# Performance work log

Hardware: AMD Instinct MI355X
Metric: run time of the kernel (lower is better)

Reference implementation:

```python
import jax, jax.numpy as jnp
import numpy as np

D_MODEL = 1024
NUM_HEADS = 16
D_K = D_MODEL // NUM_HEADS
B, S = 1, 4096


def setup_inputs() -> dict:
    key = jax.random.key(0)
    ks = jax.random.split(key, 11)
    std = 1.0 / np.sqrt(D_MODEL)
    def lin(k):
        kw, kb = jax.random.split(k)
        W = jax.random.uniform(kw, (D_MODEL, D_MODEL), jnp.float32, -std, std)
        b = jax.random.uniform(kb, (D_MODEL,), jnp.float32, -std, std)
        return W, b
    Wq, bq = lin(ks[0]); Wk, bk = lin(ks[1]); Wv, bv = lin(ks[2]); Wo, bo = lin(ks[3])
    q = jax.random.normal(ks[4], (B, S, D_MODEL), jnp.float32)
    k = jax.random.normal(ks[5], (B, S, D_MODEL), jnp.float32)
    v = jax.random.normal(ks[6], (B, S, D_MODEL), jnp.float32)
    return {"q": q, "k": k, "v": v,
            "Wq": Wq, "bq": bq, "Wk": Wk, "bk": bk,
            "Wv": Wv, "bv": bv, "Wo": Wo, "bo": bo}


def reference(q, k, v, Wq, bq, Wk, bk, Wv, bv, Wo, bo):
    Bq, Sq, _ = q.shape
    # Linear projections (torch Linear: x @ W.T + b)
    def split_heads(x):
        return x.reshape(Bq, -1, NUM_HEADS, D_K).transpose(0, 2, 1, 3)  # [B,H,S,Dk]
    query = split_heads(q @ Wq.T + bq)
    key_ = split_heads(k @ Wk.T + bk)
    value = split_heads(v @ Wv.T + bv)
    scores = jnp.einsum('bhsd,bhtd->bhst', query, key_) / jnp.sqrt(jnp.float32(D_K))
    attn = jax.nn.softmax(scores, axis=-1)  # [B,H,S,S]
    ctx = jnp.einsum('bhst,bhtd->bhsd', attn, value)
    ctx = ctx.transpose(0, 2, 1, 3).reshape(Bq, Sq, NUM_HEADS * D_K)
    return ctx @ Wo.T + bo
```

## Files before the change

kernel.cpp:

```cpp
#include <hip/hip_runtime.h>
#include <cstdint>
#include <cstddef>

#define S_LEN 4096
#define DMODEL 1024
#define NHEADS 16
#define DK 64
#define ACT (S_LEN * DMODEL)
#define WELE (DMODEL * DMODEL)

typedef __bf16 bf16;
typedef bf16  bf16x4 __attribute__((ext_vector_type(4)));
typedef bf16  bf16x8 __attribute__((ext_vector_type(8)));
typedef float f32x4  __attribute__((ext_vector_type(4)));

__device__ __forceinline__ void async16(const void* g, void* l) {
    __builtin_amdgcn_global_load_lds(
        (__attribute__((address_space(1))) void*)(uintptr_t)g,
        (__attribute__((address_space(3))) void*)(uintptr_t)l,
        16, 0, 0);
}

__device__ __forceinline__ float fast_exp2(float x) {
#if __has_builtin(__builtin_amdgcn_exp2f)
    return __builtin_amdgcn_exp2f(x);
#else
    return exp2f(x);
#endif
}

__global__ void __launch_bounds__(256) cvt7(
    const float* a0, const float* a1, const float* a2,
    const float* w0, const float* w1, const float* w2, const float* w3,
    bf16* oa0, bf16* oa1, bf16* oa2,
    bf16* ow0, bf16* ow1, bf16* ow2, bf16* ow3,
    int nA, int nB)
{
    const float* s; bf16* d; int n4;
    switch (blockIdx.y) {
        case 0: s = a0; d = oa0; n4 = nA; break;
        case 1: s = a1; d = oa1; n4 = nA; break;
        case 2: s = a2; d = oa2; n4 = nA; break;
        case 3: s = w0; d = ow0; n4 = nB; break;
        case 4: s = w1; d = ow1; n4 = nB; break;
        case 5: s = w2; d = ow2; n4 = nB; break;
        default: s = w3; d = ow3; n4 = nB; break;
    }
    int i = blockIdx.x * 256 + threadIdx.x;
    if (i < n4) {
        float4 v = ((const float4*)s)[i];
        bf16x4 r = { (bf16)v.x, (bf16)v.y, (bf16)v.z, (bf16)v.w };
        ((bf16x4*)d)[i] = r;
    }
}

__device__ __forceinline__ void gemm_core_128x128(
    const bf16* __restrict__ A, const bf16* __restrict__ B,
    bf16* As, bf16* Bs, f32x4 (&acc)[4][4],
    int m0, int n0, int wm, int wn, int K)
{
    const int tid  = threadIdx.x;
    const int wave = tid >> 6;
    const int lane = tid & 63;
    const int quad = lane >> 4;
    const int l16  = lane & 15;

    const int srow = tid >> 2;
    const int scol = (tid & 3) * 8;
    const bf16* Ag = A + (size_t)(m0 + srow) * K + scol;
    const bf16* Bg = B + (size_t)(n0 + srow) * K + scol;
    char* lA = (char*)As + wave * 1024;
    char* lB = (char*)Bs + wave * 1024;

    for (int k0 = 0; k0 < K; k0 += 32) {
        async16(Ag,                  lA);
        async16(Ag + (size_t)64 * K, lA + 4096);
        async16(Bg,                  lB);
        async16(Bg + (size_t)64 * K, lB + 4096);
        Ag += 32; Bg += 32;
        __syncthreads();

        bf16x8 af[4], bfr[4];
#pragma unroll
        for (int i = 0; i < 4; ++i)
            af[i] = *(const bf16x8*)&As[(wm + i * 16 + l16) * 32 + quad * 8];
#pragma unroll
        for (int i = 0; i < 4; ++i)
            bfr[i] = *(const bf16x8*)&Bs[(wn + i * 16 + l16) * 32 + quad * 8];

#pragma unroll
        for (int mi = 0; mi < 4; ++mi)
#pragma unroll
            for (int ni = 0; ni < 4; ++ni)
                acc[mi][ni] = __builtin_amdgcn_mfma_f32_16x16x32_bf16(
                    af[mi], bfr[ni], acc[mi][ni], 0, 0, 0);
        __syncthreads();
    }
}

__global__ void __launch_bounds__(256) proj_qkv(
    const bf16* __restrict__ Xq, const bf16* __restrict__ Wq, const float* __restrict__ bq, bf16* __restrict__ Qo,
    const bf16* __restrict__ Xk, const bf16* __restrict__ Wk, const float* __restrict__ bk, bf16* __restrict__ Ko,
    const bf16* __restrict__ Xv, const bf16* __restrict__ Wv, const float* __restrict__ bv, bf16* __restrict__ Vo,
    float qscale)
{
    __shared__ __align__(16) bf16 SM[8192];

    const int which = blockIdx.z;
    const bf16*  A    = (which == 0) ? Xq : (which == 1) ? Xk : Xv;
    const bf16*  Bw   = (which == 0) ? Wq : (which == 1) ? Wk : Wv;
    const float* bias = (which == 0) ? bq : (which == 1) ? bk : bv;
    const float  scale = (which == 0) ? qscale : 1.0f;

    const int tid  = threadIdx.x;
    const int wave = tid >> 6;
    const int lane = tid & 63;
    const int quad = lane >> 4;
    const int l16  = lane & 15;
    const int m0 = blockIdx.x * 128;
    const int n0 = blockIdx.y * 128;
    const int wm = (wave & 1) * 64;
    const int wn = (wave >> 1) * 64;

    f32x4 acc[4][4] = {};
    gemm_core_128x128(A, Bw, SM, SM + 4096, acc, m0, n0, wm, wn, DMODEL);

    if (which < 2) {
        bf16* out = (which == 0) ? Qo : Ko;
        const size_t hb0 = (size_t)(n0 >> 6) * S_LEN * DK;
#pragma unroll
        for (int p = 0; p < 2; ++p) {
            if ((wave & 1) == p) {
#pragma unroll
                for (int mi = 0; mi < 4; ++mi)
#pragma unroll
                    for (int ni = 0; ni < 4; ++ni) {
                        const int nl = wn + ni * 16 + l16;
                        const float bn = bias[n0 + nl];
#pragma unroll
                        for (int r = 0; r < 4; ++r) {
                            const int row = mi * 16 + quad * 4 + r;
                            const int pos = ((((nl >> 3) ^ (row & 7)) << 3) | (nl & 7));
                            SM[row * 128 + pos] = (bf16)((acc[mi][ni][r] + bn) * scale);
                        }
                    }
            }
            __syncthreads();
#pragma unroll
            for (int j = 0; j < 4; ++j) {
                const int i = j * 256 + tid;
                const int row = i >> 4, cs = i & 15;
                bf16x8 val = *(const bf16x8*)&SM[row * 128 + cs * 8];
                const size_t dst = hb0 + (size_t)(cs >> 3) * ((size_t)S_LEN * DK)
                                 + (size_t)(m0 + p * 64 + row) * DK + (cs & 7) * 8;
                *(bf16x8*)&out[dst] = val;
            }
            __syncthreads();
        }
    } else {
#pragma unroll
        for (int mi = 0; mi < 4; ++mi)
#pragma unroll
            for (int ni = 0; ni < 4; ++ni) {
                const int n = n0 + wn + ni * 16 + l16;
                const float bn = bias[n];
                const int dk = n & 63;
                const size_t hb = (size_t)(n >> 6) * (64 * S_LEN);
                const int mbase = m0 + wm + mi * 16 + quad * 4;
                const int T  = mbase >> 6;
                const int tt = mbase & 63;
                const int pos = (((tt >> 3) ^ (dk & 7)) << 3) | (tt & 7);
                bf16x4 r4;
#pragma unroll
                for (int r = 0; r < 4; ++r) r4[r] = (bf16)(acc[mi][ni][r] + bn);
                *(bf16x4*)&Vo[hb + (size_t)T * 4096 + dk * 64 + pos] = r4;
            }
    }
}

__global__ void __launch_bounds__(256) gemm_out(
    const bf16* __restrict__ A, const bf16* __restrict__ Bw,
    const float* __restrict__ bias, float* __restrict__ out)
{
    __shared__ __align__(16) bf16 As[64 * 32];
    __shared__ __align__(16) bf16 Bs[128 * 32];

    const int tid  = threadIdx.x;
    const int wave = tid >> 6;
    const int lane = tid & 63;
    const int quad = lane >> 4;
    const int l16  = lane & 15;
    const int m0 = blockIdx.x * 64;
    const int n0 = blockIdx.y * 128;
    const int wm = (wave & 1) * 32;
    const int wn = (wave >> 1) * 64;

    const int srow = tid >> 2;
    const int scol = (tid & 3) * 8;
    const bf16* Ag  = A  + (size_t)(m0 + srow) * DMODEL + scol;
    const bf16* Bg  = Bw + (size_t)(n0 + srow) * DMODEL + scol;
    const bf16* Bg2 = Bg + (size_t)64 * DMODEL;

    f32x4 acc[2][4] = {};
    for (int k0 = 0; k0 < DMODEL; k0 += 32) {
        async16(Ag,  (char*)As + wave * 1024);
        async16(Bg,  (char*)Bs + wave * 1024);
        async16(Bg2, (char*)Bs + 4096 + wave * 1024);
        Ag += 32; Bg += 32; Bg2 += 32;
        __syncthreads();

        bf16x8 af[2], bfr[4];
#pragma unroll
        for (int i = 0; i < 2; ++i)
            af[i] = *(const bf16x8*)&As[(wm + i * 16 + l16) * 32 + quad * 8];
#pragma unroll
        for (int i = 0; i < 4; ++i)
            bfr[i] = *(const bf16x8*)&Bs[(wn + i * 16 + l16) * 32 + quad * 8];

#pragma unroll
        for (int mi = 0; mi < 2; ++mi)
#pragma unroll
            for (int ni = 0; ni < 4; ++ni)
                acc[mi][ni] = __builtin_amdgcn_mfma_f32_16x16x32_bf16(
                    af[mi], bfr[ni], acc[mi][ni], 0, 0, 0);
        __syncthreads();
    }

#pragma unroll
    for (int mi = 0; mi < 2; ++mi)
#pragma unroll
        for (int ni = 0; ni < 4; ++ni) {
            const int n = n0 + wn + ni * 16 + l16;
            const float bn = bias[n];
#pragma unroll
            for (int r = 0; r < 4; ++r) {
                const int m = m0 + wm + mi * 16 + quad * 4 + r;
                out[(size_t)m * DMODEL + n] = acc[mi][ni][r] + bn;
            }
        }
}

__global__ void __launch_bounds__(128) flash_attn(
    const bf16* __restrict__ Q, const bf16* __restrict__ Kh,
    const bf16* __restrict__ Vt, bf16* __restrict__ ctx)
{
    __shared__ __align__(16) bf16 Ks[64 * 64];
    __shared__ __align__(16) bf16 Vs[64 * 64];
    __shared__ __align__(16) bf16 Ps[2][32 * 68];

    const int tid  = threadIdx.x;
    const int wave = tid >> 6;
    const int lane = tid & 63;
    const int quad = lane >> 4;
    const int l16  = lane & 15;
    const int key8  = (quad ^ (l16 & 7)) << 3;
    const int key8b = key8 ^ 32;
    const int s0 = blockIdx.x * 64;
    const int h  = blockIdx.y;

    bf16x8 aq[2][2];
#pragma unroll
    for (int mi = 0; mi < 2; ++mi) {
        const bf16* qrow = Q + (size_t)h * S_LEN * DK
                         + (size_t)(s0 + wave * 32 + mi * 16 + l16) * DK;
        aq[mi][0] = *(const bf16x8*)(qrow + key8);
        aq[mi][1] = *(const bf16x8*)(qrow + key8b);
    }

    const bf16* Kg = Kh + (size_t)h * S_LEN * DK + tid * 8;
    const bf16* Vg = Vt + (size_t)h * (64 * S_LEN) + tid * 8;

    f32x4 o[2][4] = {};
    f32x4 lsum4[2] = {};
    bf16* Pw = &Ps[wave][0];

    for (int it = 0; it < 64; ++it) {
#pragma unroll
        for (int j = 0; j < 4; ++j) {
            async16(Kg + j * 1024, (char*)Ks + wave * 1024 + j * 2048);
            async16(Vg + j * 1024, (char*)Vs + wave * 1024 + j * 2048);
        }
        Kg += 4096; Vg += 4096;
        __syncthreads();

        f32x4 sc[2][4] = {};
#pragma unroll
        for (int ti = 0; ti < 4; ++ti) {
            const bf16* kp = &Ks[(ti * 16 + l16) * 64];
            bf16x8 bk0 = *(const bf16x8*)(kp + key8);
            bf16x8 bk1 = *(const bf16x8*)(kp + key8b);
#pragma unroll
            for (int mi = 0; mi < 2; ++mi) {
                sc[mi][ti] = __builtin_amdgcn_mfma_f32_16x16x32_bf16(bk0, aq[mi][0], sc[mi][ti], 0, 0, 0);
                sc[mi][ti] = __builtin_amdgcn_mfma_f32_16x16x32_bf16(bk1, aq[mi][1], sc[mi][ti], 0, 0, 0);
            }
        }

#pragma unroll
        for (int mi = 0; mi < 2; ++mi) {
            const int prow = (mi * 16 + l16) * 68;
#pragma unroll
            for (int ti = 0; ti < 4; ++ti) {
                f32x4 p;
#pragma unroll
                for (int r = 0; r < 4; ++r)
                    p[r] = fast_exp2(sc[mi][ti][r]);
                lsum4[mi] += p;
                bf16x4 pk = { (bf16)p[0], (bf16)p[1], (bf16)p[2], (bf16)p[3] };
                *(bf16x4*)&Pw[prow + ti * 16 + quad * 4] = pk;
            }
        }

#pragma unroll
        for (int mi = 0; mi < 2; ++mi) {
            const bf16* pb = &Pw[(mi * 16 + l16) * 68];
            bf16x4 p0a = *(const bf16x4*)(pb + quad * 8);
            bf16x4 p0b = *(const bf16x4*)(pb + quad * 8 + 4);
            bf16x4 p1a = *(const bf16x4*)(pb + 32 + quad * 8);
            bf16x4 p1b = *(const bf16x4*)(pb + 32 + quad * 8 + 4);
            bf16x8 ap0 = __builtin_shufflevector(p0a, p0b, 0, 1, 2, 3, 4, 5, 6, 7);
            bf16x8 ap1 = __builtin_shufflevector(p1a, p1b, 0, 1, 2, 3, 4, 5, 6, 7);
#pragma unroll
            for (int di = 0; di < 4; ++di) {
                const bf16* vp = &Vs[(di * 16 + l16) * 64];
                bf16x8 bv0 = *(const bf16x8*)(vp + key8);
                bf16x8 bv1 = *(const bf16x8*)(vp + key8b);
                o[mi][di] = __builtin_amdgcn_mfma_f32_16x16x32_bf16(bv0, ap0, o[mi][di], 0, 0, 0);
                o[mi][di] = __builtin_amdgcn_mfma_f32_16x16x32_bf16(bv1, ap1, o[mi][di], 0, 0, 0);
            }
        }
        __syncthreads();
    }

#pragma unroll
    for (int mi = 0; mi < 2; ++mi) {
        float ls = lsum4[mi][0] + lsum4[mi][1] + lsum4[mi][2] + lsum4[mi][3];
        ls += __shfl_xor(ls, 16);
        ls += __shfl_xor(ls, 32);
        const float rinv = 1.0f / ls;
        const int s = s0 + wave * 32 + mi * 16 + l16;
#pragma unroll
        for (int di = 0; di < 4; ++di) {
            bf16x4 r4 = { (bf16)(o[mi][di][0] * rinv), (bf16)(o[mi][di][1] * rinv),
                          (bf16)(o[mi][di][2] * rinv), (bf16)(o[mi][di][3] * rinv) };
            *(bf16x4*)&ctx[(size_t)s * DMODEL + h * DK + di * 16 + quad * 4] = r4;
        }
    }
}

extern "C" void kernel_launch(void* const* d_in, const int* in_sizes, int n_in,
                              void* d_out, int out_size, void* d_ws, size_t ws_size,
                              hipStream_t stream)
{
    (void)in_sizes; (void)n_in; (void)out_size; (void)ws_size;
    const float* q  = (const float*)d_in[0];
    const float* k  = (const float*)d_in[1];
    const float* v  = (const float*)d_in[2];
    const float* Wq = (const float*)d_in[3];
    const float* bq = (const float*)d_in[4];
    const float* Wk = (const float*)d_in[5];
    const float* bk = (const float*)d_in[6];
    const float* Wv = (const float*)d_in[7];
    const float* bv = (const float*)d_in[8];
    const float* Wo = (const float*)d_in[9];
    const float* bo = (const float*)d_in[10];

    bf16* Xq  = (bf16*)d_ws;
    bf16* Xk  = Xq  + ACT;
    bf16* Xv  = Xk  + ACT;
    bf16* Wqb = Xv  + ACT;
    bf16* Wkb = Wqb + WELE;
    bf16* Wvb = Wkb + WELE;
    bf16* Wob = Wvb + WELE;
    bf16* Qh  = Wob + WELE;
    bf16* Kh  = Qh  + ACT;
    bf16* Vt  = Kh  + ACT;
    bf16* CTX = Vt  + ACT;

    cvt7<<<dim3(ACT / 4 / 256, 7), 256, 0, stream>>>(
        q, k, v, Wq, Wk, Wv, Wo,
        Xq, Xk, Xv, Wqb, Wkb, Wvb, Wob, ACT / 4, WELE / 4);

    const float qscale = 0.125f * 1.4426950408889634f;
    proj_qkv<<<dim3(S_LEN / 128, DMODEL / 128, 3), 256, 0, stream>>>(
        Xq, Wqb, bq, Qh, Xk, Wkb, bk, Kh, Xv, Wvb, bv, Vt, qscale);

    flash_attn<<<dim3(S_LEN / 64, NHEADS), 128, 0, stream>>>(Qh, Kh, Vt, CTX);

    gemm_out<<<dim3(S_LEN / 64, DMODEL / 128), 256, 0, stream>>>(CTX, Wob, bo, (float*)d_out);
}
```

Measured before the change: 296.9 us.

## Deepen projection K-tile, scatter Q/K directly, and widen attention blocks to 128 rows

The QKV projection GEMM now loads a 64-deep K slice per barrier pair, halving the number of synchronisations. Its Q/K epilogue writes swizzled bf16 scalars straight to global memory instead of staging through LDS. The attention kernel runs 4 waves covering 128 query rows per block, so each K/V tile loaded into LDS is shared by twice as many rows, and Q is staged through LDS. The trade-offs are more LDS per block, possibly lower occupancy, and the scattered 2-byte global stores in the projection epilogue.

```diff
diff --git a/kernel.cpp b/kernel.cpp
--- a/kernel.cpp
+++ b/kernel.cpp
@@ -54,7 +54,26 @@
     }
 }
 
-__device__ __forceinline__ void gemm_core_128x128(
+__device__ __forceinline__ void gemm_compute_128(
+    const bf16* As, const bf16* Bs, f32x4 (&acc)[4][4],
+    int wm, int wn, int l16, int quad)
+{
+    bf16x8 af[4], bfr[4];
+#pragma unroll
+    for (int i = 0; i < 4; ++i)
+        af[i] = *(const bf16x8*)&As[(wm + i * 16 + l16) * 32 + quad * 8];
+#pragma unroll
+    for (int i = 0; i < 4; ++i)
+        bfr[i] = *(const bf16x8*)&Bs[(wn + i * 16 + l16) * 32 + quad * 8];
+#pragma unroll
+    for (int mi = 0; mi < 4; ++mi)
+#pragma unroll
+        for (int ni = 0; ni < 4; ++ni)
+            acc[mi][ni] = __builtin_amdgcn_mfma_f32_16x16x32_bf16(
+                af[mi], bfr[ni], acc[mi][ni], 0, 0, 0);
+}
+
+__device__ __forceinline__ void gemm_core_bk64(
     const bf16* __restrict__ A, const bf16* __restrict__ B,
     bf16* As, bf16* Bs, f32x4 (&acc)[4][4],
     int m0, int n0, int wm, int wn, int K)
@@ -72,28 +91,20 @@
     char* lA = (char*)As + wave * 1024;
     char* lB = (char*)Bs + wave * 1024;
 
-    for (int k0 = 0; k0 < K; k0 += 32) {
-        async16(Ag,                  lA);
-        async16(Ag + (size_t)64 * K, lA + 4096);
-        async16(Bg,                  lB);
-        async16(Bg + (size_t)64 * K, lB + 4096);
-        Ag += 32; Bg += 32;
-        __syncthreads();
-
-        bf16x8 af[4], bfr[4];
-#pragma unroll
-        for (int i = 0; i < 4; ++i)
-            af[i] = *(const bf16x8*)&As[(wm + i * 16 + l16) * 32 + quad * 8];
-#pragma unroll
-        for (int i = 0; i < 4; ++i)
-            bfr[i] = *(const bf16x8*)&Bs[(wn + i * 16 + l16) * 32 + quad * 8];
-
-#pragma unroll
-        for (int mi = 0; mi < 4; ++mi)
-#pragma unroll
-            for (int ni = 0; ni < 4; ++ni)
-                acc[mi][ni] = __builtin_amdgcn_mfma_f32_16x16x32_bf16(
-                    af[mi], bfr[ni], acc[mi][ni], 0, 0, 0);
+    for (int k0 = 0; k0 < K; k0 += 64) {
+        async16(Ag,                       lA);
+        async16(Ag + (size_t)64 * K,      lA + 4096);
+        async16(Ag + 32,                  lA + 8192);
+        async16(Ag + 32 + (size_t)64 * K, lA + 12288);
+        async16(Bg,                       lB);
+        async16(Bg + (size_t)64 * K,      lB + 4096);
+        async16(Bg + 32,                  lB + 8192);
+        async16(Bg + 32 + (size_t)64 * K, lB + 12288);
+        Ag += 64; Bg += 64;
+        __syncthreads();
+
+        gemm_compute_128(As,        Bs,        acc, wm, wn, l16, quad);
+        gemm_compute_128(As + 4096, Bs + 4096, acc, wm, wn, l16, quad);
         __syncthreads();
     }
 }
@@ -104,7 +115,8 @@
     const bf16* __restrict__ Xv, const bf16* __restrict__ Wv, const float* __restrict__ bv, bf16* __restrict__ Vo,
     float qscale)
 {
-    __shared__ __align__(16) bf16 SM[8192];
+    __shared__ __align__(16) bf16 As[2 * 128 * 32];
+    __shared__ __align__(16) bf16 Bs[2 * 128 * 32];
 
     const int which = blockIdx.z;
     const bf16*  A    = (which == 0) ? Xq : (which == 1) ? Xk : Xv;
@@ -123,40 +135,26 @@
     const int wn = (wave >> 1) * 64;
 
     f32x4 acc[4][4] = {};
-    gemm_core_128x128(A, Bw, SM, SM + 4096, acc, m0, n0, wm, wn, DMODEL);
+    gemm_core_bk64(A, Bw, As, Bs, acc, m0, n0, wm, wn, DMODEL);
 
     if (which < 2) {
         bf16* out = (which == 0) ? Qo : Ko;
-        const size_t hb0 = (size_t)(n0 >> 6) * S_LEN * DK;
-#pragma unroll
-        for (int p = 0; p < 2; ++p) {
-            if ((wave & 1) == p) {
-#pragma unroll
-                for (int mi = 0; mi < 4; ++mi)
-#pragma unroll
-                    for (int ni = 0; ni < 4; ++ni) {
-                        const int nl = wn + ni * 16 + l16;
-                        const float bn = bias[n0 + nl];
-#pragma unroll
-                        for (int r = 0; r < 4; ++r) {
-                            const int row = mi * 16 + quad * 4 + r;
-                            const int pos = ((((nl >> 3) ^ (row & 7)) << 3) | (nl & 7));
-                            SM[row * 128 + pos] = (bf16)((acc[mi][ni][r] + bn) * scale);
-                        }
-                    }
-            }
-            __syncthreads();
-#pragma unroll
-            for (int j = 0; j < 4; ++j) {
-                const int i = j * 256 + tid;
-                const int row = i >> 4, cs = i & 15;
-                bf16x8 val = *(const bf16x8*)&SM[row * 128 + cs * 8];
-                const size_t dst = hb0 + (size_t)(cs >> 3) * ((size_t)S_LEN * DK)
-                                 + (size_t)(m0 + p * 64 + row) * DK + (cs & 7) * 8;
-                *(bf16x8*)&out[dst] = val;
-            }
-            __syncthreads();
-        }
+#pragma unroll
+        for (int mi = 0; mi < 4; ++mi)
+#pragma unroll
+            for (int ni = 0; ni < 4; ++ni) {
+                const int n = n0 + wn + ni * 16 + l16;
+                const float bn = bias[n];
+                const int dk = n & 63;
+                const int cc = dk >> 3, ee = dk & 7;
+                const size_t hb = (size_t)(n >> 6) * S_LEN * DK;
+#pragma unroll
+                for (int r = 0; r < 4; ++r) {
+                    const int m = m0 + wm + mi * 16 + quad * 4 + r;
+                    const int pdk = ((cc ^ (m & 7)) << 3) | ee;
+                    out[hb + (size_t)m * DK + pdk] = (bf16)((acc[mi][ni][r] + bn) * scale);
+                }
+            }
     } else {
 #pragma unroll
         for (int mi = 0; mi < 4; ++mi)
@@ -240,13 +238,14 @@
         }
 }
 
-__global__ void __launch_bounds__(128) flash_attn(
+__global__ void __launch_bounds__(256) flash_attn(
     const bf16* __restrict__ Q, const bf16* __restrict__ Kh,
     const bf16* __restrict__ Vt, bf16* __restrict__ ctx)
 {
+    __shared__ __align__(16) bf16 Qs[128 * 64];
     __shared__ __align__(16) bf16 Ks[64 * 64];
     __shared__ __align__(16) bf16 Vs[64 * 64];
-    __shared__ __align__(16) bf16 Ps[2][32 * 68];
+    __shared__ __align__(16) bf16 Ps[4][32 * 68];
 
     const int tid  = threadIdx.x;
     const int wave = tid >> 6;
@@ -255,16 +254,23 @@
     const int l16  = lane & 15;
     const int key8  = (quad ^ (l16 & 7)) << 3;
     const int key8b = key8 ^ 32;
-    const int s0 = blockIdx.x * 64;
+    const int s0 = blockIdx.x * 128;
     const int h  = blockIdx.y;
 
+    {
+        const bf16* Qg = Q + (size_t)h * S_LEN * DK + (size_t)s0 * DK + tid * 8;
+#pragma unroll
+        for (int j = 0; j < 4; ++j)
+            async16(Qg + j * 2048, (char*)Qs + j * 4096 + wave * 1024);
+    }
+    __syncthreads();
+
     bf16x8 aq[2][2];
 #pragma unroll
     for (int mi = 0; mi < 2; ++mi) {
-        const bf16* qrow = Q + (size_t)h * S_LEN * DK
-                         + (size_t)(s0 + wave * 32 + mi * 16 + l16) * DK;
-        aq[mi][0] = *(const bf16x8*)(qrow + key8);
-        aq[mi][1] = *(const bf16x8*)(qrow + key8b);
+        const bf16* qb = &Qs[(wave * 32 + mi * 16 + l16) * 64];
+        aq[mi][0] = *(const bf16x8*)(qb + key8);
+        aq[mi][1] = *(const bf16x8*)(qb + key8b);
     }
 
     const bf16* Kg = Kh + (size_t)h * S_LEN * DK + tid * 8;
@@ -275,11 +281,10 @@
     bf16* Pw = &Ps[wave][0];
 
     for (int it = 0; it < 64; ++it) {
-#pragma unroll
-        for (int j = 0; j < 4; ++j) {
-            async16(Kg + j * 1024, (char*)Ks + wave * 1024 + j * 2048);
-            async16(Vg + j * 1024, (char*)Vs + wave * 1024 + j * 2048);
-        }
+        async16(Kg,        (char*)Ks + wave * 1024);
+        async16(Kg + 2048, (char*)Ks + 4096 + wave * 1024);
+        async16(Vg,        (char*)Vs + wave * 1024);
+        async16(Vg + 2048, (char*)Vs + 4096 + wave * 1024);
         Kg += 4096; Vg += 4096;
         __syncthreads();
 
@@ -385,7 +390,7 @@
     proj_qkv<<<dim3(S_LEN / 128, DMODEL / 128, 3), 256, 0, stream>>>(
         Xq, Wqb, bq, Qh, Xk, Wkb, bk, Kh, Xv, Wvb, bv, Vt, qscale);
 
-    flash_attn<<<dim3(S_LEN / 64, NHEADS), 128, 0, stream>>>(Qh, Kh, Vt, CTX);
+    flash_attn<<<dim3(S_LEN / 128, NHEADS), 256, 0, stream>>>(Qh, Kh, Vt, CTX);
 
     gemm_out<<<dim3(S_LEN / 64, DMODEL / 128), 256, 0, stream>>>(CTX, Wob, bo, (float*)d_out);
 }
```

New measurement: 276.1 us. 7.0% less time.
